# Kernel optimization log

Hardware: AMD Instinct MI355X
Metric: run time of the kernel (lower is better)

Reference implementation:

```python
import jax, jax.numpy as jnp
import numpy as np


def setup_inputs() -> dict:
    key = jax.random.key(0)
    k1, k2, k3 = jax.random.split(key, 3)
    B, N, D = 4096, 8192, 1024
    protein_features = jax.random.normal(k1, (B, D), dtype=jnp.float32)
    function_features = jax.random.normal(k2, (N, D), dtype=jnp.float32)
    positive_mask = jax.random.randint(k3, (B, N), 0, 2, dtype=jnp.int32)
    temperature = jnp.zeros((1,), dtype=jnp.float32)  # exp(0) = 1
    return {
        "protein_features": protein_features,
        "function_features": function_features,
        "positive_mask": positive_mask,
        "temperature": temperature,
    }


def reference(protein_features, function_features, positive_mask, temperature):
    # logits: [B, N]
    logits = jnp.matmul(protein_features, function_features.T) / jnp.exp(temperature[0])
    # row-wise logsumexp, computed ONCE per row (the torch loop recomputes it per positive)
    lse = jax.nn.logsumexp(logits, axis=1, keepdims=True)  # [B, 1]
    m = (positive_mask == 1).astype(logits.dtype)          # [B, N]
    n_pos = m.sum()
    # per-pair loss = -pos_logit + logsumexp(row); mean over all positive pairs
    loss_sum = ((lse - logits) * m).sum()
    return jnp.where(n_pos > 0, loss_sum / n_pos, jnp.zeros((), dtype=logits.dtype))
```

## Files before the change

kernel.cpp:

```cpp
#include <hip/hip_runtime.h>
#include <hip/hip_bf16.h>

typedef __attribute__((ext_vector_type(4))) float f32x4;
typedef __attribute__((ext_vector_type(8))) __bf16 bf16x8;
typedef __attribute__((ext_vector_type(8))) unsigned short u16x8;

constexpr int BROWS = 4096;
constexpr int NCOLS = 8192;
constexpr int DK    = 1024;
constexpr int BM = 128, BN = 128, BK = 32;
constexpr int NCB = NCOLS / BN;

__device__ static inline unsigned short f2bf(float f) {
  unsigned int u = __builtin_bit_cast(unsigned int, f);
  u += 0x7FFFu + ((u >> 16) & 1u);
  return (unsigned short)(u >> 16);
}

__device__ static inline void gload16(const void* g, void* l) {
  __builtin_amdgcn_global_load_lds(
      (const __attribute__((address_space(1))) void*)g,
      (__attribute__((address_space(3))) void*)l, 16, 0, 0);
}

__global__ void convert_kernel(const float* __restrict__ src,
                               unsigned short* __restrict__ dst,
                               int n4, int applyScale,
                               const float* __restrict__ temp) {
  float scale = applyScale ? expf(-temp[0]) : 1.0f;
  int i = blockIdx.x * blockDim.x + threadIdx.x;
  if (i >= n4) return;
  float4 v = reinterpret_cast<const float4*>(src)[i];
  ushort4 o;
  o.x = f2bf(v.x * scale);
  o.y = f2bf(v.y * scale);
  o.z = f2bf(v.z * scale);
  o.w = f2bf(v.w * scale);
  reinterpret_cast<ushort4*>(dst)[i] = o;
}

__global__ __launch_bounds__(256, 2)
void main_kernel(const unsigned short* __restrict__ Pb,
                 const unsigned short* __restrict__ Fb,
                 const int* __restrict__ mask,
                 f32x4* __restrict__ partials) {
  __shared__ __align__(16) unsigned short As[BM * BK];
  __shared__ __align__(16) unsigned short Bs[BN * BK];
  __shared__ float redM[2][BM];
  __shared__ float redS[2][BM];
  __shared__ float redP[2][BM];
  __shared__ float redC[2][BM];

  const int t    = threadIdx.x;
  const int lane = t & 63;
  const int w    = t >> 6;
  const int wr   = w >> 1;
  const int wc   = w & 1;
  const int l15  = lane & 15;
  const int l4   = lane >> 4;

  const int brow = blockIdx.y * BM;
  const int bcol = blockIdx.x * BN;

  f32x4 acc[4][4] = {};

  const int cA = w * 2;
  const int rowInC = lane >> 2;
  const int kInC   = (lane & 3) * 8;

  const unsigned short* Pg = Pb + (size_t)brow * DK;
  const unsigned short* Fg = Fb + (size_t)bcol * DK;

  for (int k0 = 0; k0 < DK; k0 += BK) {
    if (k0) __syncthreads();
    gload16(&Pg[(size_t)(cA * 16 + rowInC) * DK + k0 + kInC],       &As[cA * 512]);
    gload16(&Pg[(size_t)((cA + 1) * 16 + rowInC) * DK + k0 + kInC], &As[(cA + 1) * 512]);
    gload16(&Fg[(size_t)(cA * 16 + rowInC) * DK + k0 + kInC],       &Bs[cA * 512]);
    gload16(&Fg[(size_t)((cA + 1) * 16 + rowInC) * DK + k0 + kInC], &Bs[(cA + 1) * 512]);
    __syncthreads();

    bf16x8 af[4], bfr[4];
#pragma unroll
    for (int i = 0; i < 4; ++i) {
      af[i]  = __builtin_bit_cast(bf16x8,
                 *reinterpret_cast<const u16x8*>(&As[(wr * 64 + i * 16 + l15) * BK + l4 * 8]));
      bfr[i] = __builtin_bit_cast(bf16x8,
                 *reinterpret_cast<const u16x8*>(&Bs[(wc * 64 + i * 16 + l15) * BK + l4 * 8]));
    }
#pragma unroll
    for (int i = 0; i < 4; ++i)
#pragma unroll
      for (int j = 0; j < 4; ++j)
        acc[i][j] = __builtin_amdgcn_mfma_f32_16x16x32_bf16(af[i], bfr[j], acc[i][j], 0, 0, 0);
  }

#pragma unroll
  for (int i = 0; i < 4; ++i) {
#pragma unroll
    for (int r = 0; r < 4; ++r) {
      float v0 = acc[i][0][r], v1 = acc[i][1][r], v2 = acc[i][2][r], v3 = acc[i][3][r];
      float mx = fmaxf(fmaxf(v0, v1), fmaxf(v2, v3));
#pragma unroll
      for (int s = 1; s < 16; s <<= 1) mx = fmaxf(mx, __shfl_xor(mx, s, 64));
      float se = __expf(v0 - mx) + __expf(v1 - mx) + __expf(v2 - mx) + __expf(v3 - mx);

      const int lrow = wr * 64 + i * 16 + l4 * 4 + r;
      const int* mrow = mask + (size_t)(brow + lrow) * NCOLS + bcol + wc * 64 + l15;
      float ps = 0.f, pc = 0.f;
      if (mrow[0]  == 1) { ps += v0; pc += 1.f; }
      if (mrow[16] == 1) { ps += v1; pc += 1.f; }
      if (mrow[32] == 1) { ps += v2; pc += 1.f; }
      if (mrow[48] == 1) { ps += v3; pc += 1.f; }
#pragma unroll
      for (int s = 1; s < 16; s <<= 1) {
        se += __shfl_xor(se, s, 64);
        ps += __shfl_xor(ps, s, 64);
        pc += __shfl_xor(pc, s, 64);
      }
      if (l15 == 0) {
        redM[wc][lrow] = mx;
        redS[wc][lrow] = se;
        redP[wc][lrow] = ps;
        redC[wc][lrow] = pc;
      }
    }
  }
  __syncthreads();

  if (t < BM) {
    float m0 = redM[0][t], m1 = redM[1][t];
    float m  = fmaxf(m0, m1);
    float s  = redS[0][t] * __expf(m0 - m) + redS[1][t] * __expf(m1 - m);
    float ps = redP[0][t] + redP[1][t];
    float pc = redC[0][t] + redC[1][t];
    f32x4 out4;
    out4.x = m; out4.y = s; out4.z = ps; out4.w = pc;
    partials[(size_t)(brow + t) * NCB + blockIdx.x] = out4;
  }
}

__global__ void row_reduce_kernel(const f32x4* __restrict__ partials,
                                  float* __restrict__ rowContrib,
                                  float* __restrict__ rowCnt) {
  const int row  = blockIdx.x * 4 + (threadIdx.x >> 6);
  const int lane = threadIdx.x & 63;
  f32x4 p = partials[(size_t)row * NCB + lane];
  float m = p.x;
#pragma unroll
  for (int s = 1; s < 64; s <<= 1) m = fmaxf(m, __shfl_xor(m, s, 64));
  float se = p.y * __expf(p.x - m);
  float ps = p.z, pc = p.w;
#pragma unroll
  for (int s = 1; s < 64; s <<= 1) {
    se += __shfl_xor(se, s, 64);
    ps += __shfl_xor(ps, s, 64);
    pc += __shfl_xor(pc, s, 64);
  }
  if (lane == 0) {
    float lse = m + logf(se);
    rowContrib[row] = pc * lse - ps;
    rowCnt[row]     = pc;
  }
}

__global__ void final_kernel(const float* __restrict__ rowContrib,
                             const float* __restrict__ rowCnt,
                             float* __restrict__ out) {
  __shared__ double sC[256];
  __shared__ double sN[256];
  double c = 0.0, n = 0.0;
  for (int i = threadIdx.x; i < BROWS; i += 256) {
    c += (double)rowContrib[i];
    n += (double)rowCnt[i];
  }
  sC[threadIdx.x] = c;
  sN[threadIdx.x] = n;
  __syncthreads();
  for (int s = 128; s > 0; s >>= 1) {
    if ((int)threadIdx.x < s) {
      sC[threadIdx.x] += sC[threadIdx.x + s];
      sN[threadIdx.x] += sN[threadIdx.x + s];
    }
    __syncthreads();
  }
  if (threadIdx.x == 0) out[0] = (sN[0] > 0.0) ? (float)(sC[0] / sN[0]) : 0.0f;
}

extern "C" void kernel_launch(void* const* d_in, const int* in_sizes, int n_in,
                              void* d_out, int out_size, void* d_ws, size_t ws_size,
                              hipStream_t stream) {
  const float* P    = (const float*)d_in[0];
  const float* F    = (const float*)d_in[1];
  const int*   mask = (const int*)d_in[2];
  const float* temp = (const float*)d_in[3];
  float* out = (float*)d_out;

  char* ws = (char*)d_ws;
  unsigned short* Pb = (unsigned short*)ws;
  unsigned short* Fb = (unsigned short*)(ws + (size_t)BROWS * DK * 2);
  f32x4* partials    = (f32x4*)(ws + (size_t)(BROWS + NCOLS) * DK * 2);
  float* rowContrib  = (float*)((char*)partials + (size_t)BROWS * NCB * sizeof(f32x4));
  float* rowCnt      = rowContrib + BROWS;

  const int nP4 = BROWS * DK / 4;
  const int nF4 = NCOLS * DK / 4;
  hipLaunchKernelGGL(convert_kernel, dim3(nP4 / 256), dim3(256), 0, stream, P, Pb, nP4, 1, temp);
  hipLaunchKernelGGL(convert_kernel, dim3(nF4 / 256), dim3(256), 0, stream, F, Fb, nF4, 0, temp);
  hipLaunchKernelGGL(main_kernel, dim3(NCB, BROWS / BM), dim3(256), 0, stream, Pb, Fb, mask, partials);
  hipLaunchKernelGGL(row_reduce_kernel, dim3(BROWS / 4), dim3(256), 0, stream, partials, rowContrib, rowCnt);
  hipLaunchKernelGGL(final_kernel, dim3(1), dim3(256), 0, stream, rowContrib, rowCnt, out);
}
```

Before: 126.4 us.

## Use 256x256 double-buffered GEMM tiles with 8 waves and phased MFMA/load interleave

Replaces the single-buffered 128x128x32 bf16 GEMM with a 256x256x64 tile on 512 threads, double-buffered LDS, and a hand-scheduled loop. The loop interleaves async global-to-LDS loads with quarter-tile MFMA phases using barriers, waitcnt, sched_barrier and setprio. The aim is to hide load latency and raise arithmetic intensity per block. The trade-off is fewer blocks (512) and heavy LDS and register use, which may limit occupancy. The row-reduce is adjusted to 32 column partials.

```diff
diff --git a/kernel.cpp b/kernel.cpp
--- a/kernel.cpp
+++ b/kernel.cpp
@@ -8,8 +8,10 @@
 constexpr int BROWS = 4096;
 constexpr int NCOLS = 8192;
 constexpr int DK    = 1024;
-constexpr int BM = 128, BN = 128, BK = 32;
+constexpr int BM = 256, BN = 256, BK = 64;
 constexpr int NCB = NCOLS / BN;
+constexpr int NKT = DK / BK;
+constexpr int NIT = NKT / 2;
 
 __device__ static inline unsigned short f2bf(float f) {
   unsigned int u = __builtin_bit_cast(unsigned int, f);
@@ -39,73 +41,144 @@
   reinterpret_cast<ushort4*>(dst)[i] = o;
 }
 
-__global__ __launch_bounds__(256, 2)
+__device__ __forceinline__ void stage_half(const unsigned short* __restrict__ g,
+                                           unsigned short* l, int t, int kt) {
+#pragma unroll
+  for (int p = 0; p < 2; ++p) {
+    const int off = p * 8192 + t * 16;
+    const int row = off >> 7;
+    const int ke  = (off & 127) >> 1;
+    gload16(g + (size_t)row * DK + kt * 64 + ke, l + (off >> 1));
+  }
+}
+
+#define MFMA_BF16 __builtin_amdgcn_mfma_f32_16x16x32_bf16
+
+#define LDS_FRAG(base, row, kk) \
+  __builtin_bit_cast(bf16x8, *reinterpret_cast<const u16x8*>(&(base)[(row) * 64 + (kk) * 32 + l4 * 8]))
+
+#define READ_A(b, q)                                              \
+  aFr[0][0] = LDS_FRAG(As[b][wm], (2*(q)    )*16 + l15, 0);       \
+  aFr[0][1] = LDS_FRAG(As[b][wm], (2*(q)    )*16 + l15, 1);       \
+  aFr[1][0] = LDS_FRAG(As[b][wm], (2*(q) + 1)*16 + l15, 0);       \
+  aFr[1][1] = LDS_FRAG(As[b][wm], (2*(q) + 1)*16 + l15, 1);
+
+#define READ_B(b)                                                 \
+  bFr[0][0] = LDS_FRAG(Bs[b][bhB], brB +  0 + l15, 0);            \
+  bFr[0][1] = LDS_FRAG(Bs[b][bhB], brB +  0 + l15, 1);            \
+  bFr[1][0] = LDS_FRAG(Bs[b][bhB], brB + 16 + l15, 0);            \
+  bFr[1][1] = LDS_FRAG(Bs[b][bhB], brB + 16 + l15, 1);            \
+  bFr[2][0] = LDS_FRAG(Bs[b][bhB], brB + 32 + l15, 0);            \
+  bFr[2][1] = LDS_FRAG(Bs[b][bhB], brB + 32 + l15, 1);            \
+  bFr[3][0] = LDS_FRAG(Bs[b][bhB], brB + 48 + l15, 0);            \
+  bFr[3][1] = LDS_FRAG(Bs[b][bhB], brB + 48 + l15, 1);
+
+#define COMPUTE(q)                                                                  \
+  __builtin_amdgcn_s_setprio(1);                                                   \
+  _Pragma("unroll") for (int mm = 0; mm < 2; ++mm)                                  \
+  _Pragma("unroll") for (int n = 0; n < 4; ++n) {                                   \
+    acc[2*(q)+mm][n] = MFMA_BF16(aFr[mm][0], bFr[n][0], acc[2*(q)+mm][n], 0, 0, 0); \
+    acc[2*(q)+mm][n] = MFMA_BF16(aFr[mm][1], bFr[n][1], acc[2*(q)+mm][n], 0, 0, 0); \
+  }                                                                                 \
+  __builtin_amdgcn_s_setprio(0);
+
+#define PHASE_MID                                    \
+  __builtin_amdgcn_sched_barrier(0);                 \
+  __builtin_amdgcn_s_barrier();                      \
+  asm volatile("s_waitcnt lgkmcnt(0)" ::: "memory"); \
+  __builtin_amdgcn_sched_barrier(0);
+
+#define PHASE_END                                    \
+  __builtin_amdgcn_sched_barrier(0);                 \
+  __builtin_amdgcn_s_barrier();
+
+__global__ __launch_bounds__(512, 2)
 void main_kernel(const unsigned short* __restrict__ Pb,
                  const unsigned short* __restrict__ Fb,
                  const int* __restrict__ mask,
                  f32x4* __restrict__ partials) {
-  __shared__ __align__(16) unsigned short As[BM * BK];
-  __shared__ __align__(16) unsigned short Bs[BN * BK];
-  __shared__ float redM[2][BM];
-  __shared__ float redS[2][BM];
-  __shared__ float redP[2][BM];
-  __shared__ float redC[2][BM];
+  __shared__ __align__(16) unsigned short As[2][2][128 * 64];
+  __shared__ __align__(16) unsigned short Bs[2][2][128 * 64];
+  __shared__ float redM[4][256], redS[4][256], redP[4][256], redC[4][256];
 
   const int t    = threadIdx.x;
   const int lane = t & 63;
   const int w    = t >> 6;
-  const int wr   = w >> 1;
-  const int wc   = w & 1;
+  const int wm   = w >> 2;
+  const int wn   = w & 3;
   const int l15  = lane & 15;
   const int l4   = lane >> 4;
+  const int bhB  = wn >> 1;
+  const int brB  = (wn & 1) * 64;
 
   const int brow = blockIdx.y * BM;
   const int bcol = blockIdx.x * BN;
 
-  f32x4 acc[4][4] = {};
-
-  const int cA = w * 2;
-  const int rowInC = lane >> 2;
-  const int kInC   = (lane & 3) * 8;
-
-  const unsigned short* Pg = Pb + (size_t)brow * DK;
-  const unsigned short* Fg = Fb + (size_t)bcol * DK;
-
-  for (int k0 = 0; k0 < DK; k0 += BK) {
-    if (k0) __syncthreads();
-    gload16(&Pg[(size_t)(cA * 16 + rowInC) * DK + k0 + kInC],       &As[cA * 512]);
-    gload16(&Pg[(size_t)((cA + 1) * 16 + rowInC) * DK + k0 + kInC], &As[(cA + 1) * 512]);
-    gload16(&Fg[(size_t)(cA * 16 + rowInC) * DK + k0 + kInC],       &Bs[cA * 512]);
-    gload16(&Fg[(size_t)((cA + 1) * 16 + rowInC) * DK + k0 + kInC], &Bs[(cA + 1) * 512]);
-    __syncthreads();
-
-    bf16x8 af[4], bfr[4];
-#pragma unroll
-    for (int i = 0; i < 4; ++i) {
-      af[i]  = __builtin_bit_cast(bf16x8,
-                 *reinterpret_cast<const u16x8*>(&As[(wr * 64 + i * 16 + l15) * BK + l4 * 8]));
-      bfr[i] = __builtin_bit_cast(bf16x8,
-                 *reinterpret_cast<const u16x8*>(&Bs[(wc * 64 + i * 16 + l15) * BK + l4 * 8]));
-    }
-#pragma unroll
-    for (int i = 0; i < 4; ++i)
-#pragma unroll
-      for (int j = 0; j < 4; ++j)
-        acc[i][j] = __builtin_amdgcn_mfma_f32_16x16x32_bf16(af[i], bfr[j], acc[i][j], 0, 0, 0);
-  }
-
-#pragma unroll
-  for (int i = 0; i < 4; ++i) {
+  const unsigned short* Ag0 = Pb + (size_t)brow * DK;
+  const unsigned short* Ag1 = Pb + (size_t)(brow + 128) * DK;
+  const unsigned short* Bg0 = Fb + (size_t)bcol * DK;
+  const unsigned short* Bg1 = Fb + (size_t)(bcol + 128) * DK;
+
+  f32x4 acc[8][4] = {};
+  bf16x8 bFr[4][2];
+  bf16x8 aFr[2][2];
+
+  stage_half(Bg0, Bs[0][0], t, 0);
+  stage_half(Bg1, Bs[0][1], t, 0);
+  stage_half(Ag0, As[0][0], t, 0);
+  stage_half(Ag1, As[0][1], t, 0);
+  stage_half(Bg0, Bs[1][0], t, 1);
+  stage_half(Bg1, Bs[1][1], t, 1);
+  asm volatile("s_waitcnt vmcnt(4)" ::: "memory");
+  __builtin_amdgcn_sched_barrier(0);
+  __builtin_amdgcn_s_barrier();
+
+  for (int i = 0; i < NIT; ++i) {
+    const int t1 = 2 * i + 1;
+    const bool more = (i < NIT - 1);
+    READ_B(0); READ_A(0, 0);
+    stage_half(Ag0, As[1][0], t, t1);
+    PHASE_MID; COMPUTE(0); PHASE_END;
+    READ_A(0, 1);
+    stage_half(Ag1, As[1][1], t, t1);
+    PHASE_MID; COMPUTE(1); PHASE_END;
+    READ_A(0, 2);
+    if (more) stage_half(Bg0, Bs[0][0], t, t1 + 1);
+    PHASE_MID; COMPUTE(2); PHASE_END;
+    READ_A(0, 3);
+    if (more) stage_half(Bg1, Bs[0][1], t, t1 + 1);
+    PHASE_MID; COMPUTE(3);
+    if (more) { asm volatile("s_waitcnt vmcnt(4)" ::: "memory"); }
+    else      { asm volatile("s_waitcnt vmcnt(0)" ::: "memory"); }
+    PHASE_END;
+    READ_B(1); READ_A(1, 0);
+    if (more) stage_half(Ag0, As[0][0], t, t1 + 1);
+    PHASE_MID; COMPUTE(0); PHASE_END;
+    READ_A(1, 1);
+    if (more) stage_half(Ag1, As[0][1], t, t1 + 1);
+    PHASE_MID; COMPUTE(1); PHASE_END;
+    READ_A(1, 2);
+    if (more) stage_half(Bg0, Bs[1][0], t, t1 + 2);
+    PHASE_MID; COMPUTE(2); PHASE_END;
+    READ_A(1, 3);
+    if (more) stage_half(Bg1, Bs[1][1], t, t1 + 2);
+    PHASE_MID; COMPUTE(3);
+    if (more) { asm volatile("s_waitcnt vmcnt(4)" ::: "memory"); }
+    PHASE_END;
+  }
+
+#pragma unroll
+  for (int m = 0; m < 8; ++m) {
 #pragma unroll
     for (int r = 0; r < 4; ++r) {
-      float v0 = acc[i][0][r], v1 = acc[i][1][r], v2 = acc[i][2][r], v3 = acc[i][3][r];
+      float v0 = acc[m][0][r], v1 = acc[m][1][r], v2 = acc[m][2][r], v3 = acc[m][3][r];
       float mx = fmaxf(fmaxf(v0, v1), fmaxf(v2, v3));
 #pragma unroll
       for (int s = 1; s < 16; s <<= 1) mx = fmaxf(mx, __shfl_xor(mx, s, 64));
       float se = __expf(v0 - mx) + __expf(v1 - mx) + __expf(v2 - mx) + __expf(v3 - mx);
 
-      const int lrow = wr * 64 + i * 16 + l4 * 4 + r;
-      const int* mrow = mask + (size_t)(brow + lrow) * NCOLS + bcol + wc * 64 + l15;
+      const int lr = wm * 128 + m * 16 + l4 * 4 + r;
+      const int* mrow = mask + (size_t)(brow + lr) * NCOLS + bcol + wn * 64 + l15;
       float ps = 0.f, pc = 0.f;
       if (mrow[0]  == 1) { ps += v0; pc += 1.f; }
       if (mrow[16] == 1) { ps += v1; pc += 1.f; }
@@ -118,21 +191,22 @@
         pc += __shfl_xor(pc, s, 64);
       }
       if (l15 == 0) {
-        redM[wc][lrow] = mx;
-        redS[wc][lrow] = se;
-        redP[wc][lrow] = ps;
-        redC[wc][lrow] = pc;
+        redM[wn][lr] = mx;
+        redS[wn][lr] = se;
+        redP[wn][lr] = ps;
+        redC[wn][lr] = pc;
       }
     }
   }
   __syncthreads();
 
-  if (t < BM) {
-    float m0 = redM[0][t], m1 = redM[1][t];
-    float m  = fmaxf(m0, m1);
-    float s  = redS[0][t] * __expf(m0 - m) + redS[1][t] * __expf(m1 - m);
-    float ps = redP[0][t] + redP[1][t];
-    float pc = redC[0][t] + redC[1][t];
+  if (t < 256) {
+    float m0 = redM[0][t], m1 = redM[1][t], m2 = redM[2][t], m3 = redM[3][t];
+    float m  = fmaxf(fmaxf(m0, m1), fmaxf(m2, m3));
+    float s  = redS[0][t] * __expf(m0 - m) + redS[1][t] * __expf(m1 - m)
+             + redS[2][t] * __expf(m2 - m) + redS[3][t] * __expf(m3 - m);
+    float ps = redP[0][t] + redP[1][t] + redP[2][t] + redP[3][t];
+    float pc = redC[0][t] + redC[1][t] + redC[2][t] + redC[3][t];
     f32x4 out4;
     out4.x = m; out4.y = s; out4.z = ps; out4.w = pc;
     partials[(size_t)(brow + t) * NCB + blockIdx.x] = out4;
@@ -144,14 +218,14 @@
                                   float* __restrict__ rowCnt) {
   const int row  = blockIdx.x * 4 + (threadIdx.x >> 6);
   const int lane = threadIdx.x & 63;
-  f32x4 p = partials[(size_t)row * NCB + lane];
+  f32x4 p = partials[(size_t)row * NCB + (lane & 31)];
   float m = p.x;
 #pragma unroll
-  for (int s = 1; s < 64; s <<= 1) m = fmaxf(m, __shfl_xor(m, s, 64));
+  for (int s = 1; s < 32; s <<= 1) m = fmaxf(m, __shfl_xor(m, s, 64));
   float se = p.y * __expf(p.x - m);
   float ps = p.z, pc = p.w;
 #pragma unroll
-  for (int s = 1; s < 64; s <<= 1) {
+  for (int s = 1; s < 32; s <<= 1) {
     se += __shfl_xor(se, s, 64);
     ps += __shfl_xor(ps, s, 64);
     pc += __shfl_xor(pc, s, 64);
@@ -206,7 +280,7 @@
   const int nF4 = NCOLS * DK / 4;
   hipLaunchKernelGGL(convert_kernel, dim3(nP4 / 256), dim3(256), 0, stream, P, Pb, nP4, 1, temp);
   hipLaunchKernelGGL(convert_kernel, dim3(nF4 / 256), dim3(256), 0, stream, F, Fb, nF4, 0, temp);
-  hipLaunchKernelGGL(main_kernel, dim3(NCB, BROWS / BM), dim3(256), 0, stream, Pb, Fb, mask, partials);
+  hipLaunchKernelGGL(main_kernel, dim3(NCOLS / BN, BROWS / BM), dim3(512), 0, stream, Pb, Fb, mask, partials);
   hipLaunchKernelGGL(row_reduce_kernel, dim3(BROWS / 4), dim3(256), 0, stream, partials, rowContrib, rowCnt);
   hipLaunchKernelGGL(final_kernel, dim3(1), dim3(256), 0, stream, rowContrib, rowCnt, out);
 }
```

Result: slower. 135.1 us (+6.9%).

## Double-buffer GEMM tiles with BK=64, XOR-swizzled LDS and phased MFMA scheduling

Applied to the files above, without the earlier changes.

Rewrites the GEMM main loop of the fused logits/logsumexp kernel. It uses double-buffered LDS tiles with BK=64 and XOR-swizzled layouts to avoid bank conflicts. Global loads for the next K tile are issued while MFMAs on the current tile run, using explicit vmcnt waits, raw barriers and s_setprio. The goal is to hide global load latency and remove the two full syncthreads per K step. LDS use doubles to 64KB per block, which may limit occupancy to two blocks per CU.

```diff
diff --git a/kernel.cpp b/kernel.cpp
--- a/kernel.cpp
+++ b/kernel.cpp
@@ -8,8 +8,10 @@
 constexpr int BROWS = 4096;
 constexpr int NCOLS = 8192;
 constexpr int DK    = 1024;
-constexpr int BM = 128, BN = 128, BK = 32;
+constexpr int BM = 128, BN = 128, BK = 64;
 constexpr int NCB = NCOLS / BN;
+constexpr int NKT = DK / BK;
+constexpr int NIT = NKT / 2;
 
 __device__ static inline unsigned short f2bf(float f) {
   unsigned int u = __builtin_bit_cast(unsigned int, f);
@@ -39,73 +41,122 @@
   reinterpret_cast<ushort4*>(dst)[i] = o;
 }
 
+__device__ __forceinline__ void stage_tile(const unsigned short* __restrict__ g,
+                                           unsigned short* l, int t, int kt) {
+#pragma unroll
+  for (int p = 0; p < 4; ++p) {
+    const int off = p * 4096 + t * 16;
+    const int row = off >> 7;
+    const int keSw = ((off & 127) >> 1) ^ ((row & 7) << 3);
+    gload16(g + (size_t)row * DK + kt * 64 + keSw, l + (off >> 1));
+  }
+}
+
+#define MFMA_BF16 __builtin_amdgcn_mfma_f32_16x16x32_bf16
+
+#define LDS_FRAG(base, row, kk)                                             \
+  __builtin_bit_cast(bf16x8, *reinterpret_cast<const u16x8*>(               \
+      &(base)[((row) * 64 + (kk) * 32 + l4 * 8) ^ (((row) & 7) << 3)]))
+
+#define READ_A(buf, q)                                                  \
+  aFr[0][0] = LDS_FRAG(buf, wm * 64 + (2*(q)    )*16 + l15, 0);         \
+  aFr[0][1] = LDS_FRAG(buf, wm * 64 + (2*(q)    )*16 + l15, 1);         \
+  aFr[1][0] = LDS_FRAG(buf, wm * 64 + (2*(q) + 1)*16 + l15, 0);         \
+  aFr[1][1] = LDS_FRAG(buf, wm * 64 + (2*(q) + 1)*16 + l15, 1);
+
+#define READ_B(buf)                                                     \
+  bFr[0][0] = LDS_FRAG(buf, wn * 64 +  0 + l15, 0);                     \
+  bFr[0][1] = LDS_FRAG(buf, wn * 64 +  0 + l15, 1);                     \
+  bFr[1][0] = LDS_FRAG(buf, wn * 64 + 16 + l15, 0);                     \
+  bFr[1][1] = LDS_FRAG(buf, wn * 64 + 16 + l15, 1);                     \
+  bFr[2][0] = LDS_FRAG(buf, wn * 64 + 32 + l15, 0);                     \
+  bFr[2][1] = LDS_FRAG(buf, wn * 64 + 32 + l15, 1);                     \
+  bFr[3][0] = LDS_FRAG(buf, wn * 64 + 48 + l15, 0);                     \
+  bFr[3][1] = LDS_FRAG(buf, wn * 64 + 48 + l15, 1);
+
+#define COMPUTE(q)                                                                  \
+  __builtin_amdgcn_s_setprio(1);                                                   \
+  _Pragma("unroll") for (int mm = 0; mm < 2; ++mm)                                  \
+  _Pragma("unroll") for (int n = 0; n < 4; ++n) {                                   \
+    acc[2*(q)+mm][n] = MFMA_BF16(aFr[mm][0], bFr[n][0], acc[2*(q)+mm][n], 0, 0, 0); \
+    acc[2*(q)+mm][n] = MFMA_BF16(aFr[mm][1], bFr[n][1], acc[2*(q)+mm][n], 0, 0, 0); \
+  }                                                                                 \
+  __builtin_amdgcn_s_setprio(0);
+
+#define PHASE_MID                                    \
+  __builtin_amdgcn_s_barrier();                      \
+  asm volatile("s_waitcnt lgkmcnt(0)" ::: "memory");
+
+#define PHASE_END                                    \
+  __builtin_amdgcn_s_barrier();
+
 __global__ __launch_bounds__(256, 2)
 void main_kernel(const unsigned short* __restrict__ Pb,
                  const unsigned short* __restrict__ Fb,
                  const int* __restrict__ mask,
                  f32x4* __restrict__ partials) {
-  __shared__ __align__(16) unsigned short As[BM * BK];
-  __shared__ __align__(16) unsigned short Bs[BN * BK];
-  __shared__ float redM[2][BM];
-  __shared__ float redS[2][BM];
-  __shared__ float redP[2][BM];
-  __shared__ float redC[2][BM];
+  __shared__ __align__(16) unsigned short Ab[2][128 * 64];
+  __shared__ __align__(16) unsigned short Bb[2][128 * 64];
+  __shared__ float redM[2][128], redS[2][128], redP[2][128], redC[2][128];
 
   const int t    = threadIdx.x;
   const int lane = t & 63;
   const int w    = t >> 6;
-  const int wr   = w >> 1;
-  const int wc   = w & 1;
+  const int wm   = w >> 1;
+  const int wn   = w & 1;
   const int l15  = lane & 15;
   const int l4   = lane >> 4;
 
   const int brow = blockIdx.y * BM;
   const int bcol = blockIdx.x * BN;
 
+  const unsigned short* Ag = Pb + (size_t)brow * DK;
+  const unsigned short* Bg = Fb + (size_t)bcol * DK;
+
   f32x4 acc[4][4] = {};
-
-  const int cA = w * 2;
-  const int rowInC = lane >> 2;
-  const int kInC   = (lane & 3) * 8;
-
-  const unsigned short* Pg = Pb + (size_t)brow * DK;
-  const unsigned short* Fg = Fb + (size_t)bcol * DK;
-
-  for (int k0 = 0; k0 < DK; k0 += BK) {
-    if (k0) __syncthreads();
-    gload16(&Pg[(size_t)(cA * 16 + rowInC) * DK + k0 + kInC],       &As[cA * 512]);
-    gload16(&Pg[(size_t)((cA + 1) * 16 + rowInC) * DK + k0 + kInC], &As[(cA + 1) * 512]);
-    gload16(&Fg[(size_t)(cA * 16 + rowInC) * DK + k0 + kInC],       &Bs[cA * 512]);
-    gload16(&Fg[(size_t)((cA + 1) * 16 + rowInC) * DK + k0 + kInC], &Bs[(cA + 1) * 512]);
-    __syncthreads();
-
-    bf16x8 af[4], bfr[4];
-#pragma unroll
-    for (int i = 0; i < 4; ++i) {
-      af[i]  = __builtin_bit_cast(bf16x8,
-                 *reinterpret_cast<const u16x8*>(&As[(wr * 64 + i * 16 + l15) * BK + l4 * 8]));
-      bfr[i] = __builtin_bit_cast(bf16x8,
-                 *reinterpret_cast<const u16x8*>(&Bs[(wc * 64 + i * 16 + l15) * BK + l4 * 8]));
+  bf16x8 bFr[4][2];
+  bf16x8 aFr[2][2];
+
+  stage_tile(Ag, Ab[0], t, 0);
+  stage_tile(Bg, Bb[0], t, 0);
+  asm volatile("s_waitcnt vmcnt(0)" ::: "memory");
+  __builtin_amdgcn_s_barrier();
+
+  for (int j = 0; j < NIT; ++j) {
+    const int t0 = 2 * j, t1 = 2 * j + 1;
+    const bool more = (j < NIT - 1);
+    READ_B(Bb[0]); READ_A(Ab[0], 0);
+    stage_tile(Ag, Ab[1], t, t1);
+    asm volatile("s_waitcnt vmcnt(4)" ::: "memory");
+    PHASE_MID; COMPUTE(0); PHASE_END;
+    READ_A(Ab[0], 1);
+    stage_tile(Bg, Bb[1], t, t1);
+    PHASE_MID; COMPUTE(1); PHASE_END;
+    READ_B(Bb[1]); READ_A(Ab[1], 0);
+    if (more) {
+      stage_tile(Ag, Ab[0], t, t0 + 2);
+      asm volatile("s_waitcnt vmcnt(4)" ::: "memory");
+    } else {
+      asm volatile("s_waitcnt vmcnt(0)" ::: "memory");
     }
-#pragma unroll
-    for (int i = 0; i < 4; ++i)
-#pragma unroll
-      for (int j = 0; j < 4; ++j)
-        acc[i][j] = __builtin_amdgcn_mfma_f32_16x16x32_bf16(af[i], bfr[j], acc[i][j], 0, 0, 0);
-  }
-
-#pragma unroll
-  for (int i = 0; i < 4; ++i) {
+    PHASE_MID; COMPUTE(0); PHASE_END;
+    READ_A(Ab[1], 1);
+    if (more) stage_tile(Bg, Bb[0], t, t0 + 2);
+    PHASE_MID; COMPUTE(1); PHASE_END;
+  }
+
+#pragma unroll
+  for (int m = 0; m < 4; ++m) {
 #pragma unroll
     for (int r = 0; r < 4; ++r) {
-      float v0 = acc[i][0][r], v1 = acc[i][1][r], v2 = acc[i][2][r], v3 = acc[i][3][r];
+      float v0 = acc[m][0][r], v1 = acc[m][1][r], v2 = acc[m][2][r], v3 = acc[m][3][r];
       float mx = fmaxf(fmaxf(v0, v1), fmaxf(v2, v3));
 #pragma unroll
       for (int s = 1; s < 16; s <<= 1) mx = fmaxf(mx, __shfl_xor(mx, s, 64));
       float se = __expf(v0 - mx) + __expf(v1 - mx) + __expf(v2 - mx) + __expf(v3 - mx);
 
-      const int lrow = wr * 64 + i * 16 + l4 * 4 + r;
-      const int* mrow = mask + (size_t)(brow + lrow) * NCOLS + bcol + wc * 64 + l15;
+      const int lr = wm * 64 + m * 16 + l4 * 4 + r;
+      const int* mrow = mask + (size_t)(brow + lr) * NCOLS + bcol + wn * 64 + l15;
       float ps = 0.f, pc = 0.f;
       if (mrow[0]  == 1) { ps += v0; pc += 1.f; }
       if (mrow[16] == 1) { ps += v1; pc += 1.f; }
@@ -118,16 +169,16 @@
         pc += __shfl_xor(pc, s, 64);
       }
       if (l15 == 0) {
-        redM[wc][lrow] = mx;
-        redS[wc][lrow] = se;
-        redP[wc][lrow] = ps;
-        redC[wc][lrow] = pc;
+        redM[wn][lr] = mx;
+        redS[wn][lr] = se;
+        redP[wn][lr] = ps;
+        redC[wn][lr] = pc;
       }
     }
   }
   __syncthreads();
 
-  if (t < BM) {
+  if (t < 128) {
     float m0 = redM[0][t], m1 = redM[1][t];
     float m  = fmaxf(m0, m1);
     float s  = redS[0][t] * __expf(m0 - m) + redS[1][t] * __expf(m1 - m);
@@ -206,7 +257,7 @@
   const int nF4 = NCOLS * DK / 4;
   hipLaunchKernelGGL(convert_kernel, dim3(nP4 / 256), dim3(256), 0, stream, P, Pb, nP4, 1, temp);
   hipLaunchKernelGGL(convert_kernel, dim3(nF4 / 256), dim3(256), 0, stream, F, Fb, nF4, 0, temp);
-  hipLaunchKernelGGL(main_kernel, dim3(NCB, BROWS / BM), dim3(256), 0, stream, Pb, Fb, mask, partials);
+  hipLaunchKernelGGL(main_kernel, dim3(NCOLS / BN, BROWS / BM), dim3(256), 0, stream, Pb, Fb, mask, partials);
   hipLaunchKernelGGL(row_reduce_kernel, dim3(BROWS / 4), dim3(256), 0, stream, partials, rowContrib, rowCnt);
   hipLaunchKernelGGL(final_kernel, dim3(1), dim3(256), 0, stream, rowContrib, rowCnt, out);
 }
```

Result: slower. 129.2 us (+2.2%).
